# Kernel optimization log

Measured on AMD Instinct MI355X. Metric: run time of the kernel, lower is better.

## Reference

```python
import jax, jax.numpy as jnp
import numpy as np

N_NODES = 50000
IN_DIM = 128
N_HID = 128
K = 4
ROUTIT = 3
N_LAYER = 2
TAU = 1.0


def setup_inputs() -> dict:
    key = jax.random.key(0)
    k1, k2, k3, k4, k5, k6 = jax.random.split(key, 6)
    feat = jax.random.normal(k1, (N_NODES, IN_DIM), dtype=jnp.float32)
    edge_index = jax.random.randint(k2, (2, 800000), 0, N_NODES, dtype=jnp.int64)
    # nn.Linear-style params (stored as [in, out] for x @ W + b)
    lin_w = jax.random.normal(k3, (IN_DIM, N_HID), dtype=jnp.float32) / np.sqrt(IN_DIM)
    lin_b = jax.random.normal(k4, (N_HID,), dtype=jnp.float32) * 0.01
    mlp_w = jax.random.normal(k5, (N_HID, N_HID), dtype=jnp.float32) / np.sqrt(N_HID)
    mlp_b = jax.random.normal(k6, (N_HID,), dtype=jnp.float32) * 0.01
    return {"feat": feat, "edge_index": edge_index, "lin_w": lin_w,
            "lin_b": lin_b, "mlp_w": mlp_w, "mlp_b": mlp_b}


def _channel_normalize(x, n, k, dd):
    # F.normalize over each of the k channels (eps matches torch default 1e-12)
    v = x.reshape(n, k, dd)
    nrm = jnp.linalg.norm(v, axis=2, keepdims=True)
    return (v / jnp.maximum(nrm, 1e-12)).reshape(n, k * dd)


def _routing_layer(x, src, trg):
    n, d = x.shape
    m = src.shape[0]
    dd = d // K
    x = _channel_normalize(x, n, K, dd)
    z = x[src].reshape(m, K, dd)  # gather per-edge source features
    c = x
    for t in range(ROUTIT):
        # Faithful to torch: c[trg].view(m, dd, K) is a reshape, NOT a transpose.
        # matmul(z, c_reshaped).sum(-1) == einsum over dd with c_reshaped summed over its trailing K.
        s = c[trg].reshape(m, dd, K).sum(axis=-1)          # [m, dd]
        p = jnp.einsum('mka,ma->mk', z, s)                 # [m, K]
        p = jax.nn.softmax(p / TAU, axis=1)
        weight_sum = (p[:, :, None] * z).reshape(m, d)     # [m, d]
        c = jax.ops.segment_sum(weight_sum, trg, num_segments=n) + x
        if t < ROUTIT - 1:
            c = _channel_normalize(c, n, K, dd)
    return c


def reference(feat, edge_index, lin_w, lin_b, mlp_w, mlp_b):
    src = edge_index[0]
    trg = edge_index[1]
    x = feat @ lin_w + lin_b
    for _ in range(N_LAYER):
        x = _routing_layer(x, src, trg)
    out = x @ mlp_w + mlp_b
    return (out, x)
```

## Files before the change

### kernel.cpp

```cpp
#include <hip/hip_runtime.h>

#define NN 50000
#define ND (NN * 128)
#define SCAN_B 49
#define CAP 16
#define LOG2E 1.4426950408889634f

typedef float f32x2 __attribute__((ext_vector_type(2)));

#if defined(__has_builtin)
#  if __has_builtin(__builtin_amdgcn_exp2f)
#    define EXP2F(x) __builtin_amdgcn_exp2f(x)
#  else
#    define EXP2F(x) exp2f(x)
#  endif
#else
#  define EXP2F(x) exp2f(x)
#endif

__device__ __forceinline__ float b2f(unsigned short u) {
    union { unsigned int i; float f; } v; v.i = ((unsigned int)u) << 16; return v.f;
}
__device__ __forceinline__ unsigned short f2b(float f) {
    union { float f; unsigned int i; } v; v.f = f;
    return (unsigned short)((v.i + 0x7fffu + ((v.i >> 16) & 1u)) >> 16);
}
__device__ __forceinline__ unsigned int pack2(float lo, float hi) {
    return (unsigned int)f2b(lo) | ((unsigned int)f2b(hi) << 16);
}
__device__ __forceinline__ float unlo(unsigned int u) { return __uint_as_float(u << 16); }
__device__ __forceinline__ float unhi(unsigned int u) { return __uint_as_float(u & 0xFFFF0000u); }
__device__ __forceinline__ int clampi(int i, int lo, int hi) { return max(lo, min(i, hi)); }

template<int CTRL>
__device__ __forceinline__ float dmov(float v) {
    return __int_as_float(__builtin_amdgcn_update_dpp(0, __float_as_int(v), CTRL, 0xF, 0xF, true));
}
template<int CTRL> __device__ __forceinline__ float dadd(float v) { return v + dmov<CTRL>(v); }
__device__ __forceinline__ float qsum(float v) { v = dadd<0xB1>(v); v = dadd<0x4E>(v); return v; }
__device__ __forceinline__ float rsum4(float v) { v = dadd<0x124>(v); v = dadd<0x128>(v); return v; }

__global__ __launch_bounds__(256) void detect(
    const unsigned short* __restrict__ feat_u, const unsigned int* __restrict__ ei_u,
    int* __restrict__ flags)
{
    int tid = threadIdx.x;
    int f32hit = 0;
    for (int i = tid; i < 8192; i += 256) {
        unsigned e = (feat_u[i] >> 7) & 0xFFu;
        if (e >= 0xC0u) f32hit = 1;
    }
    int i32hit = 0;
    for (int i = tid; i < 4096; i += 256)
        if (ei_u[2 * i + 1] != 0u) i32hit = 1;
    if (f32hit) atomicOr(&flags[0], 1);
    if (i32hit) atomicOr(&flags[1], 1);
}

__global__ __launch_bounds__(256) void prep_w(
    const void* __restrict__ W1, const void* __restrict__ B1,
    const void* __restrict__ W2, const void* __restrict__ B2,
    float* __restrict__ w1o, float* __restrict__ b1o,
    float* __restrict__ w2o, float* __restrict__ b2o,
    const int* __restrict__ flags)
{
    bool isF32 = flags[0] != 0;
    int idx = blockIdx.x * 256 + threadIdx.x;
    if (idx < 16384) {
        if (isF32) { w1o[idx] = ((const float*)W1)[idx]; w2o[idx] = ((const float*)W2)[idx]; }
        else {
            w1o[idx] = b2f(((const unsigned short*)W1)[idx]);
            w2o[idx] = b2f(((const unsigned short*)W2)[idx]);
        }
    }
    if (idx < 128) {
        if (isF32) { b1o[idx] = ((const float*)B1)[idx]; b2o[idx] = ((const float*)B2)[idx]; }
        else {
            b1o[idx] = b2f(((const unsigned short*)B1)[idx]);
            b2o[idx] = b2f(((const unsigned short*)B2)[idx]);
        }
    }
}

__global__ __launch_bounds__(256) void conv_hist(
    const void* __restrict__ eiRaw, int* __restrict__ srcA, int* __restrict__ trgA,
    int* __restrict__ deg, int m, const int* __restrict__ flags)
{
    int e = blockIdx.x * 256 + threadIdx.x;
    if (e >= m) return;
    int src, trg;
    if (flags[1]) { const int* p = (const int*)eiRaw; src = p[e]; trg = p[m + e]; }
    else { const long long* p = (const long long*)eiRaw; src = (int)p[e]; trg = (int)p[m + e]; }
    src = clampi(src, 0, NN - 1);
    trg = clampi(trg, 0, NN - 1);
    srcA[e] = src; trgA[e] = trg;
    atomicAdd(&deg[trg], 1);
}

__global__ __launch_bounds__(256) void scan1(
    const int* __restrict__ deg, int* __restrict__ rowStart, int* __restrict__ blkSum)
{
    __shared__ int lds[256];
    int blk = blockIdx.x, tid = threadIdx.x;
    int base = blk * 1024 + tid * 4;
    int v[4]; int s = 0;
    #pragma unroll
    for (int j = 0; j < 4; ++j) { int idx = base + j; v[j] = (idx < NN) ? deg[idx] : 0; s += v[j]; }
    lds[tid] = s; __syncthreads();
    for (int off = 1; off < 256; off <<= 1) {
        int x = (tid >= off) ? lds[tid - off] : 0;
        __syncthreads();
        lds[tid] += x;
        __syncthreads();
    }
    int excl = lds[tid] - s;
    if (tid == 255) blkSum[blk] = lds[tid];
    int run = excl;
    #pragma unroll
    for (int j = 0; j < 4; ++j) { int idx = base + j; if (idx < NN) rowStart[idx] = run; run += v[j]; }
}
__global__ __launch_bounds__(64) void scan2(
    int* __restrict__ blkSum, int* __restrict__ blkOff, int* __restrict__ rowStart, int m)
{
    int lane = threadIdx.x;
    int orig = (lane < SCAN_B) ? blkSum[lane] : 0;
    int v = orig;
    for (int off = 1; off < 64; off <<= 1) {
        int x = __shfl_up(v, off);
        if (lane >= off) v += x;
    }
    if (lane < SCAN_B) blkOff[lane] = v - orig;
    if (lane == 0) rowStart[NN] = m;
}
__global__ __launch_bounds__(256) void scan3(
    int* __restrict__ rowStart, const int* __restrict__ blkOff, int* __restrict__ cursor)
{
    int base = blockIdx.x * 1024 + threadIdx.x * 4;
    int off = blkOff[blockIdx.x];
    #pragma unroll
    for (int j = 0; j < 4; ++j) {
        int idx = base + j;
        if (idx < NN) { int v = rowStart[idx] + off; rowStart[idx] = v; cursor[idx] = v; }
    }
}

__global__ __launch_bounds__(256) void scatter_csr(
    const int* __restrict__ srcA, const int* __restrict__ trgA,
    int* __restrict__ cursor, int* __restrict__ eSrc, int m)
{
    int e = blockIdx.x * 256 + threadIdx.x;
    if (e >= m) return;
    int pos = atomicAdd(&cursor[trgA[e]], 1);
    eSrc[pos] = srcA[e];
}

__global__ __launch_bounds__(256) void gemm_norm(
    const void* __restrict__ A, const float* __restrict__ W, const float* __restrict__ bias,
    unsigned short* __restrict__ XNh, const int* __restrict__ flags)
{
    __shared__ float As[32 * 128];
    int tid = threadIdx.x;
    int cg = tid & 31;
    int rg = tid >> 5;
    int rowBase = blockIdx.x * 32;
    bool isF32 = flags[0] != 0;

    #pragma unroll
    for (int r = 0; r < 4; ++r) {
        int lrow = r * 8 + rg;
        int row = rowBase + lrow;
        float4 v = make_float4(0.f, 0.f, 0.f, 0.f);
        if (row < NN) {
            if (isF32) v = *(const float4*)&((const float*)A)[(long)row * 128 + cg * 4];
            else {
                ushort4 u = *(const ushort4*)&((const unsigned short*)A)[(long)row * 128 + cg * 4];
                v = make_float4(b2f(u.x), b2f(u.y), b2f(u.z), b2f(u.w));
            }
        }
        *(float4*)&As[lrow * 128 + cg * 4] = v;
    }
    float4 bb = *(const float4*)&bias[cg * 4];
    __syncthreads();

    float acc[4][4];
    #pragma unroll
    for (int i = 0; i < 4; ++i) { acc[i][0]=bb.x; acc[i][1]=bb.y; acc[i][2]=bb.z; acc[i][3]=bb.w; }

    #pragma unroll 2
    for (int k4 = 0; k4 < 32; ++k4) {
        float4 w[4], av[4];
        #pragma unroll
        for (int j = 0; j < 4; ++j)
            w[j] = *(const float4*)&W[(k4 * 4 + j) * 128 + cg * 4];
        #pragma unroll
        for (int i = 0; i < 4; ++i)
            av[i] = *(const float4*)&As[(rg * 4 + i) * 128 + k4 * 4];
        #pragma unroll
        for (int i = 0; i < 4; ++i) {
            const float a0 = av[i].x, a1 = av[i].y, a2 = av[i].z, a3 = av[i].w;
            acc[i][0] = fmaf(a0, w[0].x, fmaf(a1, w[1].x, fmaf(a2, w[2].x, fmaf(a3, w[3].x, acc[i][0]))));
            acc[i][1] = fmaf(a0, w[0].y, fmaf(a1, w[1].y, fmaf(a2, w[2].y, fmaf(a3, w[3].y, acc[i][1]))));
            acc[i][2] = fmaf(a0, w[0].z, fmaf(a1, w[1].z, fmaf(a2, w[2].z, fmaf(a3, w[3].z, acc[i][2]))));
            acc[i][3] = fmaf(a0, w[0].w, fmaf(a1, w[1].w, fmaf(a2, w[2].w, fmaf(a3, w[3].w, acc[i][3]))));
        }
    }
    #pragma unroll
    for (int i = 0; i < 4; ++i) {
        int row = rowBase + rg * 4 + i;
        float lss = acc[i][0]*acc[i][0] + acc[i][1]*acc[i][1] + acc[i][2]*acc[i][2] + acc[i][3]*acc[i][3];
        lss += __shfl_xor(lss, 1);
        lss += __shfl_xor(lss, 2);
        lss += __shfl_xor(lss, 4);
        float scale = 1.0f / fmaxf(sqrtf(lss), 1e-12f);
        if (row < NN) {
            float4 o; o.x = acc[i][0]*scale; o.y = acc[i][1]*scale; o.z = acc[i][2]*scale; o.w = acc[i][3]*scale;
            uint2 pk; pk.x = pack2(o.x, o.y); pk.y = pack2(o.z, o.w);
            *(uint2*)((char*)XNh + (long)row * 256 + cg * 8) = pk;
        }
    }
}

__global__ __launch_bounds__(256) void gemm_plain(
    const float* __restrict__ A, const float* __restrict__ W, const float* __restrict__ bias,
    float* __restrict__ Out)
{
    __shared__ float As[32 * 128];
    int tid = threadIdx.x;
    int cg = tid & 31;
    int rg = tid >> 5;
    int rowBase = blockIdx.x * 32;

    #pragma unroll
    for (int r = 0; r < 4; ++r) {
        int lrow = r * 8 + rg;
        int row = rowBase + lrow;
        float4 v = make_float4(0.f, 0.f, 0.f, 0.f);
        if (row < NN) v = *(const float4*)&A[(long)row * 128 + cg * 4];
        *(float4*)&As[lrow * 128 + cg * 4] = v;
    }
    float4 bb = *(const float4*)&bias[cg * 4];
    __syncthreads();

    float acc[4][4];
    #pragma unroll
    for (int i = 0; i < 4; ++i) { acc[i][0]=bb.x; acc[i][1]=bb.y; acc[i][2]=bb.z; acc[i][3]=bb.w; }

    #pragma unroll 2
    for (int k4 = 0; k4 < 32; ++k4) {
        float4 w[4], av[4];
        #pragma unroll
        for (int j = 0; j < 4; ++j)
            w[j] = *(const float4*)&W[(k4 * 4 + j) * 128 + cg * 4];
        #pragma unroll
        for (int i = 0; i < 4; ++i)
            av[i] = *(const float4*)&As[(rg * 4 + i) * 128 + k4 * 4];
        #pragma unroll
        for (int i = 0; i < 4; ++i) {
            const float a0 = av[i].x, a1 = av[i].y, a2 = av[i].z, a3 = av[i].w;
            acc[i][0] = fmaf(a0, w[0].x, fmaf(a1, w[1].x, fmaf(a2, w[2].x, fmaf(a3, w[3].x, acc[i][0]))));
            acc[i][1] = fmaf(a0, w[0].y, fmaf(a1, w[1].y, fmaf(a2, w[2].y, fmaf(a3, w[3].y, acc[i][1]))));
            acc[i][2] = fmaf(a0, w[0].z, fmaf(a1, w[1].z, fmaf(a2, w[2].z, fmaf(a3, w[3].z, acc[i][2]))));
            acc[i][3] = fmaf(a0, w[0].w, fmaf(a1, w[1].w, fmaf(a2, w[2].w, fmaf(a3, w[3].w, acc[i][3]))));
        }
    }
    #pragma unroll
    for (int i = 0; i < 4; ++i) {
        int row = rowBase + rg * 4 + i;
        if (row < NN) {
            float4 o; o.x = acc[i][0]; o.y = acc[i][1]; o.z = acc[i][2]; o.w = acc[i][3];
            *(float4*)&Out[(long)row * 128 + cg * 4] = o;
        }
    }
}

#define PROC4(ZU, c0, c1, c2, c3) { \
    f32x2 za0 = {unlo(ZU.x), unhi(ZU.x)}; \
    f32x2 za1 = {unlo(ZU.y), unhi(ZU.y)}; \
    f32x2 za2 = {unlo(ZU.z), unhi(ZU.z)}; \
    f32x2 za3 = {unlo(ZU.w), unhi(ZU.w)}; \
    f32x2 dd_ = za0 * s0; \
    dd_ = __builtin_elementwise_fma(za1, s1, dd_); \
    dd_ = __builtin_elementwise_fma(za2, s2, dd_); \
    dd_ = __builtin_elementwise_fma(za3, s3, dd_); \
    float p = dd_.x + dd_.y; \
    p = qsum(p); \
    float ex = EXP2F(p); \
    float sm = rsum4(ex); \
    float wgt = ex * __builtin_amdgcn_rcpf(sm); \
    f32x2 w2 = {wgt, wgt}; \
    c0 = __builtin_elementwise_fma(w2, za0, c0); \
    c1 = __builtin_elementwise_fma(w2, za1, c1); \
    c2 = __builtin_elementwise_fma(w2, za2, c2); \
    c3 = __builtin_elementwise_fma(w2, za3, c3); }

__global__ __launch_bounds__(256) void route_layer(
    const int* __restrict__ rowStart, const int* __restrict__ eSrc,
    const unsigned short* __restrict__ XNh,
    unsigned short* __restrict__ XNOut, float* __restrict__ CT)
{
    __shared__ unsigned short zbuf[4][CAP * 128];
    int w = threadIdx.x >> 6;
    int node = blockIdx.x * 4 + w;
    int lane = threadIdx.x & 63;
    int slot = lane >> 4;
    int h = lane & 15;
    int beg = rowStart[node], end = rowStart[node + 1];
    int deg = end - beg;
    int degL = min(deg, CAP);
    const char* XNb = (const char*)XNh;

    for (int r = slot; r < degL; r += 4) {
        int src = eSrc[beg + r];
        uint4 v = *(const uint4*)(XNb + (src * 256 + h * 16));
        *(uint4*)&zbuf[w][r * 128 + h * 8] = v;
    }
    uint4 xr = *(const uint4*)(XNb + (node * 256 + h * 16));
    float x0 = unlo(xr.x), x1 = unhi(xr.x), x2 = unlo(xr.y), x3 = unhi(xr.y);
    float x4 = unlo(xr.z), x5 = unhi(xr.z), x6 = unlo(xr.w), x7 = unhi(xr.w);
    float tx = (x0 + x1 + x2 + x3) * LOG2E;
    float ty = (x4 + x5 + x6 + x7) * LOG2E;
    int sb = (lane & 48) | (4 * (h & 3));
    f32x2 s0, s1, s2, s3;
    s0.x = __shfl(tx, sb);     s0.y = __shfl(ty, sb);
    s1.x = __shfl(tx, sb + 1); s1.y = __shfl(ty, sb + 1);
    s2.x = __shfl(tx, sb + 2); s2.y = __shfl(ty, sb + 2);
    s3.x = __shfl(tx, sb + 3); s3.y = __shfl(ty, sb + 3);
    asm volatile("s_waitcnt lgkmcnt(0)" ::: "memory");

    f32x2 a0, a1, a2, a3;
    #pragma unroll
    for (int iter = 0; iter < 3; ++iter) {
        if (slot == 0) {
            a0 = (f32x2){x0, x1}; a1 = (f32x2){x2, x3};
            a2 = (f32x2){x4, x5}; a3 = (f32x2){x6, x7};
        } else {
            a0 = (f32x2){0.f, 0.f}; a1 = a0; a2 = a0; a3 = a0;
        }
        f32x2 b0 = (f32x2){0.f, 0.f}, b1 = b0, b2 = b0, b3 = b0;
        int i = slot;
        for (; i + 4 < degL; i += 8) {
            uint4 zu0 = *(const uint4*)&zbuf[w][i * 128 + h * 8];
            uint4 zu1 = *(const uint4*)&zbuf[w][(i + 4) * 128 + h * 8];
            PROC4(zu0, a0, a1, a2, a3);
            PROC4(zu1, b0, b1, b2, b3);
        }
        if (i < degL) {
            uint4 zu = *(const uint4*)&zbuf[w][i * 128 + h * 8];
            PROC4(zu, a0, a1, a2, a3);
        }
        for (int j = CAP + slot; j < deg; j += 4) {
            uint4 zu = *(const uint4*)(XNb + (eSrc[beg + j] * 256 + h * 16));
            PROC4(zu, b0, b1, b2, b3);
        }
        a0 += b0; a1 += b1; a2 += b2; a3 += b3;
        a0.x += __shfl_xor(a0.x, 16); a0.x += __shfl_xor(a0.x, 32);
        a0.y += __shfl_xor(a0.y, 16); a0.y += __shfl_xor(a0.y, 32);
        a1.x += __shfl_xor(a1.x, 16); a1.x += __shfl_xor(a1.x, 32);
        a1.y += __shfl_xor(a1.y, 16); a1.y += __shfl_xor(a1.y, 32);
        a2.x += __shfl_xor(a2.x, 16); a2.x += __shfl_xor(a2.x, 32);
        a2.y += __shfl_xor(a2.y, 16); a2.y += __shfl_xor(a2.y, 32);
        a3.x += __shfl_xor(a3.x, 16); a3.x += __shfl_xor(a3.x, 32);
        a3.y += __shfl_xor(a3.y, 16); a3.y += __shfl_xor(a3.y, 32);
        if (iter < 2) {
            f32x2 q = a0 * a0;
            q = __builtin_elementwise_fma(a1, a1, q);
            q = __builtin_elementwise_fma(a2, a2, q);
            q = __builtin_elementwise_fma(a3, a3, q);
            float ssq = qsum(q.x + q.y);
            float scl = LOG2E / fmaxf(sqrtf(ssq), 1e-12f);
            tx = (a0.x + a0.y + a1.x + a1.y) * scl;
            ty = (a2.x + a2.y + a3.x + a3.y) * scl;
            s0.x = __shfl(tx, sb);     s0.y = __shfl(ty, sb);
            s1.x = __shfl(tx, sb + 1); s1.y = __shfl(ty, sb + 1);
            s2.x = __shfl(tx, sb + 2); s2.y = __shfl(ty, sb + 2);
            s3.x = __shfl(tx, sb + 3); s3.y = __shfl(ty, sb + 3);
        }
    }
    if (XNOut) {
        f32x2 q = a0 * a0;
        q = __builtin_elementwise_fma(a1, a1, q);
        q = __builtin_elementwise_fma(a2, a2, q);
        q = __builtin_elementwise_fma(a3, a3, q);
        float ssq = qsum(q.x + q.y);
        float scale = 1.0f / fmaxf(sqrtf(ssq), 1e-12f);
        if (slot == 0) {
            uint4 pk;
            pk.x = pack2(a0.x * scale, a0.y * scale);
            pk.y = pack2(a1.x * scale, a1.y * scale);
            pk.z = pack2(a2.x * scale, a2.y * scale);
            pk.w = pack2(a3.x * scale, a3.y * scale);
            *(uint4*)((char*)XNOut + (node * 256 + h * 16)) = pk;
        }
    }
    if (CT && slot == 0) {
        float4* cp = (float4*)(CT + (node * 128 + 8 * h));
        cp[0] = make_float4(a0.x, a0.y, a1.x, a1.y);
        cp[1] = make_float4(a2.x, a2.y, a3.x, a3.y);
    }
}

extern "C" void kernel_launch(void* const* d_in, const int* in_sizes, int n_in,
                              void* d_out, int out_size, void* d_ws, size_t ws_size,
                              hipStream_t stream) {
    const void* feat  = d_in[0];
    const void* ei    = d_in[1];
    const void* lin_w = d_in[2];
    const void* lin_b = d_in[3];
    const void* mlp_w = d_in[4];
    const void* mlp_b = d_in[5];
    float* out = (float*)d_out;

    const int m = in_sizes[1] / 2;

    char* wsB = (char*)d_ws;
    int*   flags = (int*)wsB;
    unsigned short* XH1 = (unsigned short*)(wsB + 256);
    unsigned short* XH2 = XH1 + ND;
    int*   srcA  = (int*)(XH2 + ND);
    int*   trgA  = srcA + m;
    int*   eSrc  = trgA + m;
    int*   deg   = eSrc + m;
    int*   rowStart = deg + NN;
    int*   cursor   = rowStart + NN + 1;
    int*   blkSum   = cursor + NN;
    int*   blkOff   = blkSum + 64;
    float* W1f      = (float*)(blkOff + 64);
    float* B1f      = W1f + 16384;
    float* W2f      = B1f + 128;
    float* B2f      = W2f + 16384;

    hipMemsetAsync(flags, 0, 8, stream);
    hipMemsetAsync(deg, 0, NN * sizeof(int), stream);
    detect<<<1, 256, 0, stream>>>((const unsigned short*)feat, (const unsigned int*)ei, flags);
    prep_w<<<64, 256, 0, stream>>>(lin_w, lin_b, mlp_w, mlp_b, W1f, B1f, W2f, B2f, flags);

    const int edgeBlocks = (m + 255) / 256;
    conv_hist<<<edgeBlocks, 256, 0, stream>>>(ei, srcA, trgA, deg, m, flags);
    scan1<<<SCAN_B, 256, 0, stream>>>(deg, rowStart, blkSum);
    scan2<<<1, 64, 0, stream>>>(blkSum, blkOff, rowStart, m);
    scan3<<<SCAN_B, 256, 0, stream>>>(rowStart, blkOff, cursor);
    scatter_csr<<<edgeBlocks, 256, 0, stream>>>(srcA, trgA, cursor, eSrc, m);

    const int gemmBlocks = (NN + 31) / 32;
    const int nodeBlocks = NN / 4;

    gemm_norm<<<gemmBlocks, 256, 0, stream>>>(feat, W1f, B1f, XH1, flags);

    route_layer<<<nodeBlocks, 256, 0, stream>>>(rowStart, eSrc, XH1, XH2, nullptr);
    route_layer<<<nodeBlocks, 256, 0, stream>>>(rowStart, eSrc, XH2, nullptr, out + ND);

    gemm_plain<<<gemmBlocks, 256, 0, stream>>>(out + ND, W2f, B2f, out);
}
```

Measured before the change: 407.4 us.

## Trim CSR build launches, drop edge staging buffers, raise LDS edge cap

The two memsets are folded into the detect and prep_w kernels, and scan2 is merged into scan3 so that each block recomputes the block-offset prefix itself. The srcA/trgA staging arrays are removed: conv_hist reads only targets, and scatter_csr re-reads the raw edge_index. CAP rises from 16 to 20, so more edges per node are staged in LDS. The route_layer loop drops its second accumulator set and merges into one, which lengthens the FMA dependency chain. Together these aim to cut launch count and memory traffic in preprocessing, at the cost of less ILP and more LDS use.

```diff
diff --git a/kernel.cpp b/kernel.cpp
--- a/kernel.cpp
+++ b/kernel.cpp
@@ -3,7 +3,7 @@
 #define NN 50000
 #define ND (NN * 128)
 #define SCAN_B 49
-#define CAP 16
+#define CAP 20
 #define LOG2E 1.4426950408889634f
 
 typedef float f32x2 __attribute__((ext_vector_type(2)));
@@ -45,6 +45,8 @@
     int* __restrict__ flags)
 {
     int tid = threadIdx.x;
+    if (tid == 0) { flags[0] = 0; flags[1] = 0; }
+    __syncthreads();
     int f32hit = 0;
     for (int i = tid; i < 8192; i += 256) {
         unsigned e = (feat_u[i] >> 7) & 0xFFu;
@@ -62,7 +64,7 @@
     const void* __restrict__ W2, const void* __restrict__ B2,
     float* __restrict__ w1o, float* __restrict__ b1o,
     float* __restrict__ w2o, float* __restrict__ b2o,
-    const int* __restrict__ flags)
+    int* __restrict__ deg, const int* __restrict__ flags)
 {
     bool isF32 = flags[0] != 0;
     int idx = blockIdx.x * 256 + threadIdx.x;
@@ -80,11 +82,74 @@
             b2o[idx] = b2f(((const unsigned short*)B2)[idx]);
         }
     }
+    for (int i = idx; i < NN; i += 64 * 256) deg[i] = 0;
 }
 
 __global__ __launch_bounds__(256) void conv_hist(
-    const void* __restrict__ eiRaw, int* __restrict__ srcA, int* __restrict__ trgA,
-    int* __restrict__ deg, int m, const int* __restrict__ flags)
+    const void* __restrict__ eiRaw, int* __restrict__ deg, int m,
+    const int* __restrict__ flags)
+{
+    int e = blockIdx.x * 256 + threadIdx.x;
+    if (e >= m) return;
+    int trg;
+    if (flags[1]) trg = ((const int*)eiRaw)[m + e];
+    else          trg = (int)((const long long*)eiRaw)[m + e];
+    trg = clampi(trg, 0, NN - 1);
+    atomicAdd(&deg[trg], 1);
+}
+
+__global__ __launch_bounds__(256) void scan1(
+    const int* __restrict__ deg, int* __restrict__ rowStart, int* __restrict__ blkSum)
+{
+    __shared__ int lds[256];
+    int blk = blockIdx.x, tid = threadIdx.x;
+    int base = blk * 1024 + tid * 4;
+    int v[4]; int s = 0;
+    #pragma unroll
+    for (int j = 0; j < 4; ++j) { int idx = base + j; v[j] = (idx < NN) ? deg[idx] : 0; s += v[j]; }
+    lds[tid] = s; __syncthreads();
+    for (int off = 1; off < 256; off <<= 1) {
+        int x = (tid >= off) ? lds[tid - off] : 0;
+        __syncthreads();
+        lds[tid] += x;
+        __syncthreads();
+    }
+    int excl = lds[tid] - s;
+    if (tid == 255) blkSum[blk] = lds[tid];
+    int run = excl;
+    #pragma unroll
+    for (int j = 0; j < 4; ++j) { int idx = base + j; if (idx < NN) rowStart[idx] = run; run += v[j]; }
+}
+
+__global__ __launch_bounds__(256) void scan3(
+    int* __restrict__ rowStart, const int* __restrict__ blkSum,
+    int* __restrict__ cursor, int m)
+{
+    __shared__ int soff;
+    int tid = threadIdx.x;
+    if (tid < 64) {
+        int orig = (tid < SCAN_B) ? blkSum[tid] : 0;
+        int v = orig;
+        for (int off = 1; off < 64; off <<= 1) {
+            int x = __shfl_up(v, off);
+            if (tid >= off) v += x;
+        }
+        if (tid == (int)blockIdx.x) soff = v - orig;
+        if (blockIdx.x == 0 && tid == 0) rowStart[NN] = m;
+    }
+    __syncthreads();
+    int off = soff;
+    int base = blockIdx.x * 1024 + tid * 4;
+    #pragma unroll
+    for (int j = 0; j < 4; ++j) {
+        int idx = base + j;
+        if (idx < NN) { int v = rowStart[idx] + off; rowStart[idx] = v; cursor[idx] = v; }
+    }
+}
+
+__global__ __launch_bounds__(256) void scatter_csr(
+    const void* __restrict__ eiRaw, int* __restrict__ cursor, int* __restrict__ eSrc,
+    int m, const int* __restrict__ flags)
 {
     int e = blockIdx.x * 256 + threadIdx.x;
     if (e >= m) return;
@@ -93,65 +158,8 @@
     else { const long long* p = (const long long*)eiRaw; src = (int)p[e]; trg = (int)p[m + e]; }
     src = clampi(src, 0, NN - 1);
     trg = clampi(trg, 0, NN - 1);
-    srcA[e] = src; trgA[e] = trg;
-    atomicAdd(&deg[trg], 1);
-}
-
-__global__ __launch_bounds__(256) void scan1(
-    const int* __restrict__ deg, int* __restrict__ rowStart, int* __restrict__ blkSum)
-{
-    __shared__ int lds[256];
-    int blk = blockIdx.x, tid = threadIdx.x;
-    int base = blk * 1024 + tid * 4;
-    int v[4]; int s = 0;
-    #pragma unroll
-    for (int j = 0; j < 4; ++j) { int idx = base + j; v[j] = (idx < NN) ? deg[idx] : 0; s += v[j]; }
-    lds[tid] = s; __syncthreads();
-    for (int off = 1; off < 256; off <<= 1) {
-        int x = (tid >= off) ? lds[tid - off] : 0;
-        __syncthreads();
-        lds[tid] += x;
-        __syncthreads();
-    }
-    int excl = lds[tid] - s;
-    if (tid == 255) blkSum[blk] = lds[tid];
-    int run = excl;
-    #pragma unroll
-    for (int j = 0; j < 4; ++j) { int idx = base + j; if (idx < NN) rowStart[idx] = run; run += v[j]; }
-}
-__global__ __launch_bounds__(64) void scan2(
-    int* __restrict__ blkSum, int* __restrict__ blkOff, int* __restrict__ rowStart, int m)
-{
-    int lane = threadIdx.x;
-    int orig = (lane < SCAN_B) ? blkSum[lane] : 0;
-    int v = orig;
-    for (int off = 1; off < 64; off <<= 1) {
-        int x = __shfl_up(v, off);
-        if (lane >= off) v += x;
-    }
-    if (lane < SCAN_B) blkOff[lane] = v - orig;
-    if (lane == 0) rowStart[NN] = m;
-}
-__global__ __launch_bounds__(256) void scan3(
-    int* __restrict__ rowStart, const int* __restrict__ blkOff, int* __restrict__ cursor)
-{
-    int base = blockIdx.x * 1024 + threadIdx.x * 4;
-    int off = blkOff[blockIdx.x];
-    #pragma unroll
-    for (int j = 0; j < 4; ++j) {
-        int idx = base + j;
-        if (idx < NN) { int v = rowStart[idx] + off; rowStart[idx] = v; cursor[idx] = v; }
-    }
-}
-
-__global__ __launch_bounds__(256) void scatter_csr(
-    const int* __restrict__ srcA, const int* __restrict__ trgA,
-    int* __restrict__ cursor, int* __restrict__ eSrc, int m)
-{
-    int e = blockIdx.x * 256 + threadIdx.x;
-    if (e >= m) return;
-    int pos = atomicAdd(&cursor[trgA[e]], 1);
-    eSrc[pos] = srcA[e];
+    int pos = atomicAdd(&cursor[trg], 1);
+    eSrc[pos] = src;
 }
 
 __global__ __launch_bounds__(256) void gemm_norm(
@@ -273,7 +281,7 @@
     }
 }
 
-#define PROC4(ZU, c0, c1, c2, c3) { \
+#define PROC(ZU) { \
     f32x2 za0 = {unlo(ZU.x), unhi(ZU.x)}; \
     f32x2 za1 = {unlo(ZU.y), unhi(ZU.y)}; \
     f32x2 za2 = {unlo(ZU.z), unhi(ZU.z)}; \
@@ -288,10 +296,10 @@
     float sm = rsum4(ex); \
     float wgt = ex * __builtin_amdgcn_rcpf(sm); \
     f32x2 w2 = {wgt, wgt}; \
-    c0 = __builtin_elementwise_fma(w2, za0, c0); \
-    c1 = __builtin_elementwise_fma(w2, za1, c1); \
-    c2 = __builtin_elementwise_fma(w2, za2, c2); \
-    c3 = __builtin_elementwise_fma(w2, za3, c3); }
+    a0 = __builtin_elementwise_fma(w2, za0, a0); \
+    a1 = __builtin_elementwise_fma(w2, za1, a1); \
+    a2 = __builtin_elementwise_fma(w2, za2, a2); \
+    a3 = __builtin_elementwise_fma(w2, za3, a3); }
 
 __global__ __launch_bounds__(256) void route_layer(
     const int* __restrict__ rowStart, const int* __restrict__ eSrc,
@@ -336,23 +344,21 @@
         } else {
             a0 = (f32x2){0.f, 0.f}; a1 = a0; a2 = a0; a3 = a0;
         }
-        f32x2 b0 = (f32x2){0.f, 0.f}, b1 = b0, b2 = b0, b3 = b0;
         int i = slot;
         for (; i + 4 < degL; i += 8) {
             uint4 zu0 = *(const uint4*)&zbuf[w][i * 128 + h * 8];
             uint4 zu1 = *(const uint4*)&zbuf[w][(i + 4) * 128 + h * 8];
-            PROC4(zu0, a0, a1, a2, a3);
-            PROC4(zu1, b0, b1, b2, b3);
+            PROC(zu0);
+            PROC(zu1);
         }
         if (i < degL) {
             uint4 zu = *(const uint4*)&zbuf[w][i * 128 + h * 8];
-            PROC4(zu, a0, a1, a2, a3);
+            PROC(zu);
         }
         for (int j = CAP + slot; j < deg; j += 4) {
             uint4 zu = *(const uint4*)(XNb + (eSrc[beg + j] * 256 + h * 16));
-            PROC4(zu, b0, b1, b2, b3);
-        }
-        a0 += b0; a1 += b1; a2 += b2; a3 += b3;
+            PROC(zu);
+        }
         a0.x += __shfl_xor(a0.x, 16); a0.x += __shfl_xor(a0.x, 32);
         a0.y += __shfl_xor(a0.y, 16); a0.y += __shfl_xor(a0.y, 32);
         a1.x += __shfl_xor(a1.x, 16); a1.x += __shfl_xor(a1.x, 32);
@@ -416,30 +422,24 @@
     int*   flags = (int*)wsB;
     unsigned short* XH1 = (unsigned short*)(wsB + 256);
     unsigned short* XH2 = XH1 + ND;
-    int*   srcA  = (int*)(XH2 + ND);
-    int*   trgA  = srcA + m;
-    int*   eSrc  = trgA + m;
+    int*   eSrc  = (int*)(XH2 + ND);
     int*   deg   = eSrc + m;
     int*   rowStart = deg + NN;
     int*   cursor   = rowStart + NN + 1;
     int*   blkSum   = cursor + NN;
-    int*   blkOff   = blkSum + 64;
-    float* W1f      = (float*)(blkOff + 64);
+    float* W1f      = (float*)(blkSum + 64);
     float* B1f      = W1f + 16384;
     float* W2f      = B1f + 128;
     float* B2f      = W2f + 16384;
 
-    hipMemsetAsync(flags, 0, 8, stream);
-    hipMemsetAsync(deg, 0, NN * sizeof(int), stream);
     detect<<<1, 256, 0, stream>>>((const unsigned short*)feat, (const unsigned int*)ei, flags);
-    prep_w<<<64, 256, 0, stream>>>(lin_w, lin_b, mlp_w, mlp_b, W1f, B1f, W2f, B2f, flags);
+    prep_w<<<64, 256, 0, stream>>>(lin_w, lin_b, mlp_w, mlp_b, W1f, B1f, W2f, B2f, deg, flags);
 
     const int edgeBlocks = (m + 255) / 256;
-    conv_hist<<<edgeBlocks, 256, 0, stream>>>(ei, srcA, trgA, deg, m, flags);
+    conv_hist<<<edgeBlocks, 256, 0, stream>>>(ei, deg, m, flags);
     scan1<<<SCAN_B, 256, 0, stream>>>(deg, rowStart, blkSum);
-    scan2<<<1, 64, 0, stream>>>(blkSum, blkOff, rowStart, m);
-    scan3<<<SCAN_B, 256, 0, stream>>>(rowStart, blkOff, cursor);
-    scatter_csr<<<edgeBlocks, 256, 0, stream>>>(srcA, trgA, cursor, eSrc, m);
+    scan3<<<SCAN_B, 256, 0, stream>>>(rowStart, blkSum, cursor, m);
+    scatter_csr<<<edgeBlocks, 256, 0, stream>>>(ei, cursor, eSrc, m, flags);
 
     const int gemmBlocks = (NN + 31) / 32;
     const int nodeBlocks = NN / 4;
```

Result: faster. 390.3 us (median of 2 runs) (-4.2%).
